# Performance work log

Hardware: AMD Instinct MI355X
Metric: run time of the kernel (lower is better)

## Reference

```python
import jax, jax.numpy as jnp
import numpy as np

HEADS = 8
DIM_HEAD = 64
EPS = 1e-4


def softmax_kernel(data, proj, is_query):
    # data: [b,h,n,d], proj: [m,d]
    data_normalizer = data.shape[-1] ** -0.25
    ratio = proj.shape[0] ** -0.5
    data_dash = jnp.einsum('bhnd,md->bhnm', data_normalizer * data, proj)
    diag = (data * data).sum(-1) * 0.5 * (data_normalizer ** 2)  # [b,h,n]
    diag = diag[..., None]
    if is_query:
        stab = jnp.max(data_dash, axis=-1, keepdims=True)
    else:
        stab = jnp.max(data_dash)
    return ratio * (jnp.exp(data_dash - diag - stab) + EPS)


def linear_attention(q, k, v):
    # q,k: [b,h,n,m], v: [b,h,n,e]
    k_cumsum = k.sum(axis=-2)  # [b,h,m]
    d_inv = 1.0 / jnp.einsum('bhnm,bhm->bhn', q, k_cumsum)
    context = jnp.einsum('bhnm,bhne->bhme', k, v)  # [b,h,m,e]
    return jnp.einsum('bhme,bhnm,bhn->bhne', context, q, d_inv)


def setup_inputs() -> dict:
    key = jax.random.key(0)
    ks = jax.random.split(key, 6)
    b, n, dim = 8, 4096, 512
    m, dh = 266, DIM_HEAD
    x = jax.random.normal(ks[0], (b, n, dim), dtype=jnp.float32)
    s = dim ** -0.5
    Wq = jax.random.normal(ks[1], (dim, dim), dtype=jnp.float32) * s
    Wk = jax.random.normal(ks[2], (dim, dim), dtype=jnp.float32) * s
    Wv = jax.random.normal(ks[3], (dim, dim), dtype=jnp.float32) * s
    Wo = jax.random.normal(ks[4], (dim, dim), dtype=jnp.float32) * s
    bo = jnp.zeros((dim,), dtype=jnp.float32)
    proj = jax.random.normal(ks[5], (m, dh), dtype=jnp.float32)
    return {"x": x, "Wq": Wq, "Wk": Wk, "Wv": Wv, "Wo": Wo, "bo": bo, "proj": proj}


def reference(x, Wq, Wk, Wv, Wv_unused=None, *, _=None, **__):
    raise NotImplementedError


def reference(x, Wq, Wk, Wv, Wo, bo, proj):
    b, n, dim = x.shape
    h, dh = HEADS, DIM_HEAD
    # Linear projections (weights stored as [in, out])
    q = (x @ Wq).reshape(b, n, h, dh).transpose(0, 2, 1, 3)  # [b,h,n,dh]
    k = (x @ Wk).reshape(b, n, h, dh).transpose(0, 2, 1, 3)
    v = (x @ Wv).reshape(b, n, h, dh).transpose(0, 2, 1, 3)
    qp = softmax_kernel(q, proj, is_query=True)   # [b,h,n,m]
    kp = softmax_kernel(k, proj, is_query=False)  # [b,h,n,m]
    out = linear_attention(qp, kp, v)             # [b,h,n,dh]
    out = out.transpose(0, 2, 1, 3).reshape(b, n, h * dh)
    return out @ Wo + bo
```

## Files before the change

kernel.cpp:

```cpp
#include <hip/hip_runtime.h>
#include <stdint.h>

#define B_ 8
#define N_ 4096
#define H_ 8
#define DH_ 64
#define DIM_ 512
#define M_ 266
#define MP_ 320
#define BH_ 64
#define BNROWS_ 32768
#define CN_ 0.35355339059327373f
#define RATIO_ 0.06131393394849658f
#define EPS_ 1e-4f
#define REPS_ (RATIO_ * EPS_)

typedef __bf16 bf16x8 __attribute__((ext_vector_type(8)));
typedef float f32x4 __attribute__((ext_vector_type(4)));

union U8 { bf16x8 v; uint4 u; uint2 u2[2]; uint16_t s[8]; };

__device__ __forceinline__ uint32_t f2bf(float f) {
  uint32_t u = __float_as_uint(f);
  u += 0x7FFFu + ((u >> 16) & 1u);
  return u >> 16;
}
__device__ __forceinline__ uint32_t pkbf(float a, float b) {
  uint32_t r;
  asm("v_cvt_pk_bf16_f32 %0, %1, %2" : "=v"(r) : "v"(a), "v"(b));
  return r;
}
__device__ __forceinline__ float bflo(uint32_t u) { return __uint_as_float(u << 16); }
__device__ __forceinline__ float bfhi(uint32_t u) { return __uint_as_float(u & 0xFFFF0000u); }
__device__ __forceinline__ void unp8(uint4 u, float* f) {
  f[0] = bflo(u.x); f[1] = bfhi(u.x); f[2] = bflo(u.y); f[3] = bfhi(u.y);
  f[4] = bflo(u.z); f[5] = bfhi(u.z); f[6] = bflo(u.w); f[7] = bfhi(u.w);
}
__device__ __forceinline__ float f4get(const float4& v, int i) {
  return ((const float*)&v)[i];
}
__device__ __forceinline__ uint32_t fenc(float f) {
  uint32_t u = __float_as_uint(f);
  return u ^ ((uint32_t)((int32_t)u >> 31) | 0x80000000u);
}
__device__ __forceinline__ float fdec(uint32_t e) {
  uint32_t u = (e & 0x80000000u) ? (e ^ 0x80000000u) : ~e;
  return __uint_as_float(u);
}
__device__ __forceinline__ int piperm(int p) {
  int tmt = p >> 4, r = p & 15;
  return 32 * (tmt >> 1) + 8 * (r >> 2) + 4 * (tmt & 1) + (r & 3);
}
__device__ __forceinline__ int phinv(int r) {
  int lo = r & 15;
  return 8 * (lo >> 2) + (lo & 3) + ((r >> 4) << 2);
}
__device__ __forceinline__ void glds16(const uint16_t* g, uint16_t* l) {
  __builtin_amdgcn_global_load_lds(
      (const __attribute__((address_space(1))) void*)g,
      (__attribute__((address_space(3))) void*)l, 16, 0, 0);
}

__global__ void init_stab(uint32_t* s) { *s = fenc(-3.4e38f); }

__global__ __launch_bounds__(256) void cast_x(const float* __restrict__ x,
                                              uint16_t* __restrict__ xb, int n4) {
  int i = blockIdx.x * 256 + threadIdx.x;
  if (i >= n4) return;
  float4 v = ((const float4*)x)[i];
  uint2 o;
  o.x = f2bf(v.x) | (f2bf(v.y) << 16);
  o.y = f2bf(v.z) | (f2bf(v.w) << 16);
  ((uint2*)xb)[i] = o;
}

__global__ __launch_bounds__(256) void cast_wt(const float* __restrict__ w,
                                               uint16_t* __restrict__ wt) {
  int i = blockIdx.x * 256 + threadIdx.x;
  int k = i >> 9, n = i & 511;
  wt[(size_t)n * 512 + k] = (uint16_t)f2bf(w[i]);
}

__global__ __launch_bounds__(256) void cast_projb(const float* __restrict__ proj,
                                                  uint16_t* __restrict__ projb) {
  int i = blockIdx.x * 256 + threadIdx.x;
  if (i >= MP_ * DH_) return;
  int p = i >> 6, d = i & 63;
  int pi = piperm(p);
  float v = (pi < M_) ? proj[pi * DH_ + d] : 0.f;
  projb[i] = (uint16_t)f2bf(v);
}

template <int EPI>
__global__ __launch_bounds__(256) void gemm_glds(const uint16_t* __restrict__ A,
                                                 const uint16_t* __restrict__ Bt,
                                                 float* __restrict__ outF,
                                                 const float* __restrict__ bias,
                                                 uint16_t* __restrict__ qb,
                                                 uint16_t* __restrict__ kbuf,
                                                 uint16_t* __restrict__ vTb) {
  __shared__ __align__(16) uint16_t As[2][128 * 32];
  __shared__ __align__(16) uint16_t Bs[2][128 * 32];
  const int t = threadIdx.x, lane = t & 63, w = t >> 6;
  const int g = lane >> 4, r16 = lane & 15;
  const int wr = (w >> 1) * 64, wc = (w & 1) * 64;
  const size_t rowA0 = (size_t)blockIdx.x * 128;
  const size_t rowB0 = (size_t)blockIdx.y * 128;
  const int K = 512;

  f32x4 acc[4][4];
#pragma unroll
  for (int i = 0; i < 4; ++i)
#pragma unroll
    for (int j = 0; j < 4; ++j) acc[i][j] = (f32x4){0.f, 0.f, 0.f, 0.f};

  auto stageG = [&](int kt, int buf) {
#pragma unroll
    for (int s = 0; s < 2; ++s) {
      const int row = w * 32 + s * 16;
      const uint16_t* ga = A + (rowA0 + row + (lane >> 2)) * (size_t)K + kt * 32 + (lane & 3) * 8;
      glds16(ga, &As[buf][row * 32]);
      const uint16_t* gb = Bt + (rowB0 + row + (lane >> 2)) * (size_t)K + kt * 32 + (lane & 3) * 8;
      glds16(gb, &Bs[buf][row * 32]);
    }
  };
  stageG(0, 0);
  for (int kt = 0; kt < 16; ++kt) {
    __syncthreads();
    if (kt + 1 < 16) stageG(kt + 1, (kt + 1) & 1);
    const uint16_t* as = As[kt & 1];
    const uint16_t* bs = Bs[kt & 1];
    bf16x8 af[4], bfr[4];
#pragma unroll
    for (int i = 0; i < 4; ++i)
      af[i] = *(const bf16x8*)&as[(wr + i * 16 + r16) * 32 + g * 8];
#pragma unroll
    for (int j = 0; j < 4; ++j)
      bfr[j] = *(const bf16x8*)&bs[(wc + j * 16 + r16) * 32 + g * 8];
#pragma unroll
    for (int i = 0; i < 4; ++i)
#pragma unroll
      for (int j = 0; j < 4; ++j)
        acc[i][j] = __builtin_amdgcn_mfma_f32_16x16x32_bf16(af[i], bfr[j], acc[i][j], 0, 0, 0);
  }
  const int region = blockIdx.y >> 2;
  const int lcolBase = (blockIdx.y & 3) * 128;
#pragma unroll
  for (int i = 0; i < 4; ++i) {
    const size_t row0 = rowA0 + wr + i * 16 + g * 4;
#pragma unroll
    for (int j = 0; j < 4; ++j) {
      if constexpr (EPI == 0) {
        const size_t col = rowB0 + wc + j * 16 + r16;
        float badd = bias ? bias[col] : 0.f;
#pragma unroll
        for (int q = 0; q < 4; ++q)
          outF[(row0 + q) * (size_t)512 + col] = acc[i][j][q] + badd;
      } else {
        const int lcol = lcolBase + wc + j * 16 + r16;
        if (region == 2) {
          int bb = (int)(row0 >> 12), n = (int)(row0 & 4095);
          int hh = lcol >> 6, e = lcol & 63;
          uint2 o;
          o.x = pkbf(acc[i][j][0], acc[i][j][1]);
          o.y = pkbf(acc[i][j][2], acc[i][j][3]);
          *(uint2*)&vTb[((size_t)((bb * 8 + hh) * 64 + e)) * 4096 + n] = o;
        } else {
          uint16_t* dst = region ? kbuf : qb;
#pragma unroll
          for (int q = 0; q < 4; ++q)
            dst[(row0 + q) * (size_t)512 + lcol] = (uint16_t)f2bf(acc[i][j][q]);
        }
      }
    }
  }
}

#define GKP_ 40
template <bool AF32, bool CBF16, bool VT>
__global__ __launch_bounds__(256) void gemm_k(const void* __restrict__ Av,
                                              const uint16_t* __restrict__ Bt,
                                              void* __restrict__ Cv,
                                              const float* __restrict__ bias,
                                              int Ndim, int Kdim, int lda) {
  __shared__ uint16_t As[2][128 * GKP_];
  __shared__ uint16_t Bs[2][128 * GKP_];
  const int t = threadIdx.x;
  const int lane = t & 63;
  const int wave = t >> 6;
  const int wr = (wave >> 1) * 64, wc = (wave & 1) * 64;
  const int g = lane >> 4, r16 = lane & 15;
  const int srow = t >> 2;
  const int skk = (t & 3) * 8;
  const size_t rowA0 = (size_t)blockIdx.x * 128;
  const size_t rowB0 = (size_t)blockIdx.y * 128;

  f32x4 acc[4][4];
#pragma unroll
  for (int i = 0; i < 4; ++i)
#pragma unroll
    for (int j = 0; j < 4; ++j) acc[i][j] = (f32x4){0.f, 0.f, 0.f, 0.f};

  const int NK = Kdim >> 5;
  auto stage = [&](int kt, int buf) {
    uint4 a0, a1;
    if constexpr (AF32) {
      const float* ga = (const float*)Av + (rowA0 + srow) * (size_t)lda + kt * 32 + skk;
      float4 x0 = *(const float4*)ga;
      float4 x1 = *(const float4*)(ga + 4);
      float4 y0 = *(const float4*)(ga + 64 * (size_t)lda);
      float4 y1 = *(const float4*)(ga + 64 * (size_t)lda + 4);
      a0.x = f2bf(x0.x) | (f2bf(x0.y) << 16);
      a0.y = f2bf(x0.z) | (f2bf(x0.w) << 16);
      a0.z = f2bf(x1.x) | (f2bf(x1.y) << 16);
      a0.w = f2bf(x1.z) | (f2bf(x1.w) << 16);
      a1.x = f2bf(y0.x) | (f2bf(y0.y) << 16);
      a1.y = f2bf(y0.z) | (f2bf(y0.w) << 16);
      a1.z = f2bf(y1.x) | (f2bf(y1.y) << 16);
      a1.w = f2bf(y1.z) | (f2bf(y1.w) << 16);
    } else {
      const uint16_t* ga = (const uint16_t*)Av + (rowA0 + srow) * (size_t)lda + kt * 32 + skk;
      a0 = *(const uint4*)ga;
      a1 = *(const uint4*)(ga + 64 * (size_t)lda);
    }
    const uint16_t* gb = Bt + (rowB0 + srow) * (size_t)Kdim + kt * 32 + skk;
    uint4 b0 = *(const uint4*)gb;
    uint4 b1 = *(const uint4*)(gb + 64 * (size_t)Kdim);
    *(uint4*)&As[buf][srow * GKP_ + skk] = a0;
    *(uint4*)&As[buf][(srow + 64) * GKP_ + skk] = a1;
    *(uint4*)&Bs[buf][srow * GKP_ + skk] = b0;
    *(uint4*)&Bs[buf][(srow + 64) * GKP_ + skk] = b1;
  };
  stage(0, 0);
  for (int kt = 0; kt < NK; ++kt) {
    __syncthreads();
    if (kt + 1 < NK) stage(kt + 1, (kt + 1) & 1);
    const uint16_t* as = As[kt & 1];
    const uint16_t* bs = Bs[kt & 1];
    bf16x8 af[4], bfr[4];
#pragma unroll
    for (int i = 0; i < 4; ++i)
      af[i] = *(const bf16x8*)&as[(wr + i * 16 + r16) * GKP_ + g * 8];
#pragma unroll
    for (int j = 0; j < 4; ++j)
      bfr[j] = *(const bf16x8*)&bs[(wc + j * 16 + r16) * GKP_ + g * 8];
#pragma unroll
    for (int i = 0; i < 4; ++i)
#pragma unroll
      for (int j = 0; j < 4; ++j)
        acc[i][j] = __builtin_amdgcn_mfma_f32_16x16x32_bf16(af[i], bfr[j], acc[i][j], 0, 0, 0);
  }
#pragma unroll
  for (int i = 0; i < 4; ++i) {
    const size_t row0 = rowA0 + wr + i * 16 + g * 4;
#pragma unroll
    for (int j = 0; j < 4; ++j) {
      const size_t col = rowB0 + wc + j * 16 + r16;
      if constexpr (VT) {
        int bb = (int)(row0 >> 12), n = (int)(row0 & 4095);
        int hh = (int)(col >> 6), e = (int)(col & 63);
        uint2 o;
        o.x = pkbf(acc[i][j][0], acc[i][j][1]);
        o.y = pkbf(acc[i][j][2], acc[i][j][3]);
        *(uint2*)&((uint16_t*)Cv)[((size_t)((bb * 8 + hh) * 64 + e)) * 4096 + n] = o;
      } else {
        float badd = bias ? bias[col] : 0.f;
#pragma unroll
        for (int q = 0; q < 4; ++q) {
          float val = acc[i][j][q] + badd;
          if constexpr (CBF16)
            ((uint16_t*)Cv)[(row0 + q) * (size_t)Ndim + col] = (uint16_t)f2bf(val);
          else
            ((float*)Cv)[(row0 + q) * (size_t)Ndim + col] = val;
        }
      }
    }
  }
}

__global__ __launch_bounds__(256) void stab2_mfma(const uint16_t* __restrict__ kb,
                                                  const uint16_t* __restrict__ projb,
                                                  uint32_t* __restrict__ stab) {
  __shared__ uint16_t kt[2][32][72];
  __shared__ float wred[4];
  const int t = threadIdx.x, lane = t & 63, w = t >> 6;
  const int g = lane >> 4, r16 = lane & 15;
  const int bh = blockIdx.x, ns = blockIdx.y;
  const int b = bh >> 3, h = bh & 7;
  bf16x8 pj[5][2];
  bool mval[5];
#pragma unroll
  for (int mt = 0; mt < 5; ++mt) {
    int m16 = mt * 64 + w * 16;
    pj[mt][0] = *(const bf16x8*)&projb[(m16 + r16) * 64 + g * 8];
    pj[mt][1] = *(const bf16x8*)&projb[(m16 + r16) * 64 + 32 + g * 8];
    mval[mt] = piperm(m16 + r16) < M_;
  }
  auto stage = [&](int it, int buf) {
    int n0 = ns * 256 + it * 32;
    int row = t >> 3, c8 = t & 7;
    *(uint4*)&kt[buf][row][c8 * 8] =
        *(const uint4*)&kb[((size_t)(b * N_ + n0 + row)) * DIM_ + h * DH_ + c8 * 8];
  };
  stage(0, 0);
  __syncthreads();
  float vmax = -3.4e38f;
  for (int it = 0; it < 8; ++it) {
    int cur = it & 1;
    if (it + 1 < 8) stage(it + 1, cur ^ 1);
    bf16x8 ka[2][2];
#pragma unroll
    for (int nsub = 0; nsub < 2; ++nsub) {
      ka[nsub][0] = *(const bf16x8*)&kt[cur][nsub * 16 + r16][g * 8];
      ka[nsub][1] = *(const bf16x8*)&kt[cur][nsub * 16 + r16][32 + g * 8];
    }
#pragma unroll
    for (int mt = 0; mt < 5; ++mt) {
#pragma unroll
      for (int nsub = 0; nsub < 2; ++nsub) {
        f32x4 c4 = (f32x4){0.f, 0.f, 0.f, 0.f};
        c4 = __builtin_amdgcn_mfma_f32_16x16x32_bf16(ka[nsub][0], pj[mt][0], c4, 0, 0, 0);
        c4 = __builtin_amdgcn_mfma_f32_16x16x32_bf16(ka[nsub][1], pj[mt][1], c4, 0, 0, 0);
        if (mval[mt])
          vmax = fmaxf(vmax, fmaxf(fmaxf(c4[0], c4[1]), fmaxf(c4[2], c4[3])));
      }
    }
    __syncthreads();
  }
#pragma unroll
  for (int off = 32; off; off >>= 1) vmax = fmaxf(vmax, __shfl_xor(vmax, off));
  if (lane == 0) wred[w] = vmax;
  __syncthreads();
  if (t == 0) {
    float m = fmaxf(fmaxf(wred[0], wred[1]), fmaxf(wred[2], wred[3]));
    atomicMax(stab, fenc(CN_ * m));
  }
}

__global__ __launch_bounds__(256) void ctx_mfma(const uint16_t* __restrict__ kb,
                                                const uint16_t* __restrict__ vTb,
                                                const uint16_t* __restrict__ projb,
                                                const uint32_t* __restrict__ stab_e,
                                                float* __restrict__ ctxp,
                                                float* __restrict__ kcump,
                                                int iters) {
  __shared__ uint16_t kt[2][32][72];
  __shared__ uint16_t vt[2][64][40];
  __shared__ float dk2[2][32];
  __shared__ uint16_t kpb[4][16][40];
  const int t = threadIdx.x, lane = t & 63, w = t >> 6;
  const int g = lane >> 4, r16 = lane & 15;
  const int mt = blockIdx.x, bh = blockIdx.y, ns = blockIdx.z;
  const int b = bh >> 3, h = bh & 7;
  const int m16 = mt * 64 + w * 16;
  const float stab = fdec(*stab_e);
  const bool mvalid = piperm(m16 + r16) < M_;
  bf16x8 pj0 = *(const bf16x8*)&projb[(m16 + r16) * 64 + g * 8];
  bf16x8 pj1 = *(const bf16x8*)&projb[(m16 + r16) * 64 + 32 + g * 8];

  auto stage = [&](int it, int buf) {
    int n0 = (ns * iters + it) * 32;
    {
      int row = t >> 3, c8 = t & 7;
      uint4 kv = *(const uint4*)&kb[((size_t)(b * N_ + n0 + row)) * DIM_ + h * DH_ + c8 * 8];
      *(uint4*)&kt[buf][row][c8 * 8] = kv;
      float f[8]; unp8(kv, f);
      float sq = f[0]*f[0]+f[1]*f[1]+f[2]*f[2]+f[3]*f[3]+f[4]*f[4]+f[5]*f[5]+f[6]*f[6]+f[7]*f[7];
      sq += __shfl_xor(sq, 1); sq += __shfl_xor(sq, 2); sq += __shfl_xor(sq, 4);
      if (c8 == 0) dk2[buf][row] = 0.5f * CN_ * CN_ * sq;
    }
    {
      int e = t >> 2, c = t & 3;
      uint4 vv = *(const uint4*)&vTb[((size_t)(bh * 64 + e)) * 4096 + n0 + c * 8];
      *(uint4*)&vt[buf][e][c * 8] = vv;
    }
  };
  f32x4 acc[4];
#pragma unroll
  for (int j = 0; j < 4; ++j) acc[j] = (f32x4){0.f, 0.f, 0.f, 0.f};
  float kcacc = 0.f;

  stage(0, 0);
  __syncthreads();
  for (int it = 0; it < iters; ++it) {
    int cur = it & 1;
    if (it + 1 < iters) stage(it + 1, cur ^ 1);
#pragma unroll
    for (int nsub = 0; nsub < 2; ++nsub) {
      bf16x8 ka0 = *(const bf16x8*)&kt[cur][nsub * 16 + r16][g * 8];
      bf16x8 ka1 = *(const bf16x8*)&kt[cur][nsub * 16 + r16][32 + g * 8];
      f32x4 c4 = (f32x4){0.f, 0.f, 0.f, 0.f};
      c4 = __builtin_amdgcn_mfma_f32_16x16x32_bf16(ka0, pj0, c4, 0, 0, 0);
      c4 = __builtin_amdgcn_mfma_f32_16x16x32_bf16(ka1, pj1, c4, 0, 0, 0);
      float4 dkv = *(const float4*)&dk2[cur][nsub * 16 + 4 * g];
      float kp[4];
#pragma unroll
      for (int q = 0; q < 4; ++q) {
        float arg = CN_ * c4[q] - f4get(dkv, q) - stab;
        float e = RATIO_ * __expf(arg) + REPS_;
        kp[q] = mvalid ? e : 0.f;
        kcacc += kp[q];
      }
      *(uint2*)&kpb[w][r16][nsub * 16 + 4 * g] = make_uint2(pkbf(kp[0], kp[1]), pkbf(kp[2], kp[3]));
    }
    U8 kq; kq.u = *(const uint4*)&kpb[w][r16][g * 8];
#pragma unroll
    for (int j = 0; j < 4; ++j) {
      U8 vf; vf.u = *(const uint4*)&vt[cur][j * 16 + r16][g * 8];
      acc[j] = __builtin_amdgcn_mfma_f32_16x16x32_bf16(kq.v, vf.v, acc[j], 0, 0, 0);
    }
    __syncthreads();
  }
#pragma unroll
  for (int j = 0; j < 4; ++j) {
    float4 o = make_float4(acc[j][0], acc[j][1], acc[j][2], acc[j][3]);
    *(float4*)&ctxp[(((size_t)ns * BH_ + bh) * 64 + j * 16 + r16) * MP_ + m16 + 4 * g] = o;
  }
  kcacc += __shfl_xor(kcacc, 16);
  kcacc += __shfl_xor(kcacc, 32);
  if (lane < 16) kcump[((size_t)ns * BH_ + bh) * MP_ + m16 + lane] = kcacc;
}

__global__ __launch_bounds__(256) void merge_kernel(const float* __restrict__ ctxp,
                                                    const float* __restrict__ kcump,
                                                    uint16_t* __restrict__ ctxgb,
                                                    float* __restrict__ kcumg,
                                                    int nsp) {
  int idx = blockIdx.x * 256 + threadIdx.x;
  const int total = BH_ * 64 * MP_;
  if (idx < total) {
    float s = 0.f;
    for (int p = 0; p < nsp; ++p) s += ctxp[(size_t)p * total + idx];
    int row = idx / MP_;
    int pos = idx - row * MP_;
    int col = (pos & ~31) + phinv(pos & 31);
    ctxgb[(size_t)row * MP_ + col] = (uint16_t)f2bf(s);
  }
  const int ktotal = BH_ * MP_;
  if (idx < ktotal) {
    float s = 0.f;
    for (int p = 0; p < nsp; ++p) s += kcump[(size_t)p * ktotal + idx];
    kcumg[idx] = s;
  }
}

__global__ __launch_bounds__(512) void attn_mfma(const uint16_t* __restrict__ qb,
                                                 const uint16_t* __restrict__ projb,
                                                 const uint16_t* __restrict__ ctxgb,
                                                 const float* __restrict__ kcumg,
                                                 uint16_t* __restrict__ attnb) {
  __shared__ uint16_t ctile[64][328];
  __shared__ uint16_t qs[128][72];
  __shared__ float kcums[MP_];
  __shared__ float dqs[128];
  __shared__ float denb[8][16];
  const int t = threadIdx.x, lane = t & 63, w = t >> 6;
  const int g = lane >> 4, r16 = lane & 15;
  const int nch = blockIdx.x, bh = blockIdx.y;
  const int b = bh >> 3, h = bh & 7;
  {
    int row = t >> 3, cb = t & 7;
#pragma unroll
    for (int cc = 0; cc < 5; ++cc) {
      int cN = cb * 40 + cc * 8;
      *(uint4*)&ctile[row][cN] = *(const uint4*)&ctxgb[((size_t)bh * 64 + row) * MP_ + cN];
    }
  }
  if (t < MP_) kcums[t] = kcumg[(size_t)bh * MP_ + t];

  for (int it = 0; it < 4; ++it) {
    const int nbase = nch * 512 + it * 128;
    __syncthreads();
    {
      int row = t >> 2, c2 = t & 3;
      float sq = 0.f;
#pragma unroll
      for (int cc = 0; cc < 2; ++cc) {
        int c8 = c2 * 2 + cc;
        uint4 qv = *(const uint4*)&qb[((size_t)(b * N_ + nbase + row)) * DIM_ + h * DH_ + c8 * 8];
        *(uint4*)&qs[row][c8 * 8] = qv;
        float f[8]; unp8(qv, f);
        sq += f[0]*f[0]+f[1]*f[1]+f[2]*f[2]+f[3]*f[3]+f[4]*f[4]+f[5]*f[5]+f[6]*f[6]+f[7]*f[7];
      }
      sq += __shfl_xor(sq, 1); sq += __shfl_xor(sq, 2);
      if (c2 == 0) dqs[row] = 0.5f * CN_ * CN_ * sq;
    }
    __syncthreads();
    bf16x8 qf0 = *(const bf16x8*)&qs[w * 16 + r16][g * 8];
    bf16x8 qf1 = *(const bf16x8*)&qs[w * 16 + r16][32 + g * 8];
    f32x4 S[18];
#pragma unroll
    for (int mt = 0; mt < 18; ++mt) {
      bf16x8 pa0 = *(const bf16x8*)&projb[(mt * 16 + r16) * 64 + g * 8];
      bf16x8 pa1 = *(const bf16x8*)&projb[(mt * 16 + r16) * 64 + 32 + g * 8];
      f32x4 c4 = (f32x4){0.f, 0.f, 0.f, 0.f};
      c4 = __builtin_amdgcn_mfma_f32_16x16x32_bf16(pa0, qf0, c4, 0, 0, 0);
      S[mt] = __builtin_amdgcn_mfma_f32_16x16x32_bf16(pa1, qf1, c4, 0, 0, 0);
    }
    float rmax = -3.4e38f;
#pragma unroll
    for (int mt = 0; mt < 18; ++mt) {
#pragma unroll
      for (int q = 0; q < 4; ++q) {
        bool val = (mt < 16) || (256 + 4 * (mt & 1) + 8 * g + q < M_);
        if (val) rmax = fmaxf(rmax, CN_ * S[mt][q]);
      }
    }
    rmax = fmaxf(rmax, __shfl_xor(rmax, 16));
    rmax = fmaxf(rmax, __shfl_xor(rmax, 32));
    const float offv = rmax + dqs[w * 16 + r16];
    float denp = 0.f;
    uint32_t pk[18][2];
#pragma unroll
    for (int mt = 0; mt < 18; ++mt) {
      float4 kc4 = *(const float4*)&kcums[mt * 16 + 4 * g];
      float qp[4];
#pragma unroll
      for (int q = 0; q < 4; ++q) {
        bool val = (mt < 16) || (256 + 4 * (mt & 1) + 8 * g + q < M_);
        float e = RATIO_ * __expf(CN_ * S[mt][q] - offv) + REPS_;
        qp[q] = val ? e : 0.f;
        denp += qp[q] * f4get(kc4, q);
      }
      pk[mt][0] = pkbf(qp[0], qp[1]);
      pk[mt][1] = pkbf(qp[2], qp[3]);
    }
    denp += __shfl_xor(denp, 16);
    denp += __shfl_xor(denp, 32);
    if (lane < 16) denb[w][lane] = denp;
    f32x4 o[4];
#pragma unroll
    for (int j = 0; j < 4; ++j) o[j] = (f32x4){0.f, 0.f, 0.f, 0.f};
#pragma unroll
    for (int s = 0; s < 9; ++s) {
      U8 af; af.u = make_uint4(pk[2 * s][0], pk[2 * s][1], pk[2 * s + 1][0], pk[2 * s + 1][1]);
#pragma unroll
      for (int j = 0; j < 4; ++j) {
        U8 cf; cf.u = *(const uint4*)&ctile[j * 16 + r16][s * 32 + g * 8];
        o[j] = __builtin_amdgcn_mfma_f32_16x16x32_bf16(af.v, cf.v, o[j], 0, 0, 0);
      }
    }
    float4 dv = *(const float4*)&denb[w][4 * g];
    float rd[4];
#pragma unroll
    for (int q = 0; q < 4; ++q) rd[q] = 1.0f / f4get(dv, q);
#pragma unroll
    for (int j = 0; j < 4; ++j) {
#pragma unroll
      for (int q = 0; q < 4; ++q) {
        float val = o[j][q] * rd[q];
        int n = nbase + w * 16 + 4 * g + q;
        attnb[((size_t)(b * N_ + n)) * DIM_ + h * DH_ + j * 16 + r16] = (uint16_t)f2bf(val);
      }
    }
  }
}

extern "C" void kernel_launch(void* const* d_in, const int* in_sizes, int n_in,
                              void* d_out, int out_size, void* d_ws, size_t ws_size,
                              hipStream_t stream) {
  const float* x = (const float*)d_in[0];
  const float* Wq = (const float*)d_in[1];
  const float* Wk = (const float*)d_in[2];
  const float* Wv = (const float*)d_in[3];
  const float* Wo = (const float*)d_in[4];
  const float* bo = (const float*)d_in[5];
  const float* proj = (const float*)d_in[6];
  float* out = (float*)d_out;

  const bool tierA = ws_size >= (size_t)95000000;
  const int NS = (tierA || ws_size >= (size_t)61000000) ? 4 : 2;

  char* ws = (char*)d_ws;
  size_t off = 0;
  auto alloc = [&](size_t bytes) {
    char* p = ws + off;
    off += (bytes + 255) & ~(size_t)255;
    return p;
  };
  uint16_t* wqkvT = (uint16_t*)alloc((size_t)1536 * 512 * 2);
  uint16_t* woT = (uint16_t*)alloc((size_t)512 * 512 * 2);
  uint16_t* projb = (uint16_t*)alloc((size_t)MP_ * DH_ * 2);
  uint16_t* vTb = (uint16_t*)alloc((size_t)BNROWS_ * DIM_ * 2);
  float* ctxp = (float*)alloc((size_t)NS * BH_ * 64 * MP_ * 4);
  float* kcump = (float*)alloc((size_t)NS * BH_ * MP_ * 4);
  uint16_t* ctxgb = (uint16_t*)alloc((size_t)BH_ * 64 * MP_ * 2);
  float* kcumg = (float*)alloc((size_t)BH_ * MP_ * 4);
  uint32_t* stab = (uint32_t*)alloc(256);
  uint16_t* xb = tierA ? (uint16_t*)alloc((size_t)BNROWS_ * DIM_ * 2) : nullptr;
  uint16_t* qb = (uint16_t*)d_out;
  uint16_t* kb = qb + (size_t)BNROWS_ * DIM_;
  uint16_t* attnb = vTb;

  init_stab<<<1, 1, 0, stream>>>(stab);
  cast_wt<<<1024, 256, 0, stream>>>(Wq, wqkvT);
  cast_wt<<<1024, 256, 0, stream>>>(Wk, wqkvT + (size_t)512 * 512);
  cast_wt<<<1024, 256, 0, stream>>>(Wv, wqkvT + (size_t)1024 * 512);
  cast_wt<<<1024, 256, 0, stream>>>(Wo, woT);
  cast_projb<<<80, 256, 0, stream>>>(proj, projb);

  if (tierA) {
    cast_x<<<16384, 256, 0, stream>>>(x, xb, BNROWS_ * DIM_ / 4);
    gemm_glds<1><<<dim3(256, 12), 256, 0, stream>>>(xb, wqkvT, nullptr, nullptr, qb, kb, vTb);
  } else {
    dim3 gg(256, 4);
    gemm_k<true, true, false><<<gg, 256, 0, stream>>>(x, wqkvT, qb, nullptr, 512, 512, 512);
    gemm_k<true, true, false><<<gg, 256, 0, stream>>>(x, wqkvT + (size_t)512 * 512, kb, nullptr, 512, 512, 512);
    gemm_k<true, false, true><<<gg, 256, 0, stream>>>(x, wqkvT + (size_t)1024 * 512, vTb, nullptr, 512, 512, 512);
  }

  stab2_mfma<<<dim3(64, 16), 256, 0, stream>>>(kb, projb, stab);
  ctx_mfma<<<dim3(5, 64, NS), 256, 0, stream>>>(kb, vTb, projb, stab, ctxp, kcump, 128 / NS);
  merge_kernel<<<5120, 256, 0, stream>>>(ctxp, kcump, ctxgb, kcumg, NS);
  attn_mfma<<<dim3(8, 64), 512, 0, stream>>>(qb, projb, ctxgb, kcumg, attnb);
  gemm_k<false, false, false><<<dim3(256, 4), 256, 0, stream>>>(attnb, woT, out, bo, 512, 512, 512);
}
```

Before: 303.1 us.

## Remap GEMM blocks per XCD, raise split count, store partial contexts in bf16

The QKV GEMM now launches as a flat grid that is remapped so each XCD gets a contiguous band of row tiles, for better L2 locality. The output projection switches from the register-staged gemm_k to the direct global-to-LDS gemm_glds kernel. The workspace-tier fallback is removed so the x-cast plus fused GEMM path always runs. The ctx split count goes up to 8, and stab2 is split finer, for more parallelism. Partial contexts are stored in bf16 to halve merge traffic, at the cost of extra rounding in the partial sums.

Result: slower. 313.1 us (+3.3%).

```diff
diff --git a/kernel.cpp b/kernel.cpp
--- a/kernel.cpp
+++ b/kernel.cpp
@@ -10,6 +10,7 @@
 #define MP_ 320
 #define BH_ 64
 #define BNROWS_ 32768
+#define NS_ 8
 #define CN_ 0.35355339059327373f
 #define RATIO_ 0.06131393394849658f
 #define EPS_ 1e-4f
@@ -104,8 +105,12 @@
   const int t = threadIdx.x, lane = t & 63, w = t >> 6;
   const int g = lane >> 4, r16 = lane & 15;
   const int wr = (w >> 1) * 64, wc = (w & 1) * 64;
-  const size_t rowA0 = (size_t)blockIdx.x * 128;
-  const size_t rowB0 = (size_t)blockIdx.y * 128;
+  const int flat = blockIdx.x;
+  const int xcd = flat & 7, jj = flat >> 3;
+  const int bx = xcd * 32 + (jj & 31);
+  const int by = jj >> 5;
+  const size_t rowA0 = (size_t)bx * 128;
+  const size_t rowB0 = (size_t)by * 128;
   const int K = 512;
 
   f32x4 acc[4][4];
@@ -143,8 +148,8 @@
       for (int j = 0; j < 4; ++j)
         acc[i][j] = __builtin_amdgcn_mfma_f32_16x16x32_bf16(af[i], bfr[j], acc[i][j], 0, 0, 0);
   }
-  const int region = blockIdx.y >> 2;
-  const int lcolBase = (blockIdx.y & 3) * 128;
+  const int region = by >> 2;
+  const int lcolBase = (by & 3) * 128;
 #pragma unroll
   for (int i = 0; i < 4; ++i) {
     const size_t row0 = rowA0 + wr + i * 16 + g * 4;
@@ -176,108 +181,6 @@
   }
 }
 
-#define GKP_ 40
-template <bool AF32, bool CBF16, bool VT>
-__global__ __launch_bounds__(256) void gemm_k(const void* __restrict__ Av,
-                                              const uint16_t* __restrict__ Bt,
-                                              void* __restrict__ Cv,
-                                              const float* __restrict__ bias,
-                                              int Ndim, int Kdim, int lda) {
-  __shared__ uint16_t As[2][128 * GKP_];
-  __shared__ uint16_t Bs[2][128 * GKP_];
-  const int t = threadIdx.x;
-  const int lane = t & 63;
-  const int wave = t >> 6;
-  const int wr = (wave >> 1) * 64, wc = (wave & 1) * 64;
-  const int g = lane >> 4, r16 = lane & 15;
-  const int srow = t >> 2;
-  const int skk = (t & 3) * 8;
-  const size_t rowA0 = (size_t)blockIdx.x * 128;
-  const size_t rowB0 = (size_t)blockIdx.y * 128;
-
-  f32x4 acc[4][4];
-#pragma unroll
-  for (int i = 0; i < 4; ++i)
-#pragma unroll
-    for (int j = 0; j < 4; ++j) acc[i][j] = (f32x4){0.f, 0.f, 0.f, 0.f};
-
-  const int NK = Kdim >> 5;
-  auto stage = [&](int kt, int buf) {
-    uint4 a0, a1;
-    if constexpr (AF32) {
-      const float* ga = (const float*)Av + (rowA0 + srow) * (size_t)lda + kt * 32 + skk;
-      float4 x0 = *(const float4*)ga;
-      float4 x1 = *(const float4*)(ga + 4);
-      float4 y0 = *(const float4*)(ga + 64 * (size_t)lda);
-      float4 y1 = *(const float4*)(ga + 64 * (size_t)lda + 4);
-      a0.x = f2bf(x0.x) | (f2bf(x0.y) << 16);
-      a0.y = f2bf(x0.z) | (f2bf(x0.w) << 16);
-      a0.z = f2bf(x1.x) | (f2bf(x1.y) << 16);
-      a0.w = f2bf(x1.z) | (f2bf(x1.w) << 16);
-      a1.x = f2bf(y0.x) | (f2bf(y0.y) << 16);
-      a1.y = f2bf(y0.z) | (f2bf(y0.w) << 16);
-      a1.z = f2bf(y1.x) | (f2bf(y1.y) << 16);
-      a1.w = f2bf(y1.z) | (f2bf(y1.w) << 16);
-    } else {
-      const uint16_t* ga = (const uint16_t*)Av + (rowA0 + srow) * (size_t)lda + kt * 32 + skk;
-      a0 = *(const uint4*)ga;
-      a1 = *(const uint4*)(ga + 64 * (size_t)lda);
-    }
-    const uint16_t* gb = Bt + (rowB0 + srow) * (size_t)Kdim + kt * 32 + skk;
-    uint4 b0 = *(const uint4*)gb;
-    uint4 b1 = *(const uint4*)(gb + 64 * (size_t)Kdim);
-    *(uint4*)&As[buf][srow * GKP_ + skk] = a0;
-    *(uint4*)&As[buf][(srow + 64) * GKP_ + skk] = a1;
-    *(uint4*)&Bs[buf][srow * GKP_ + skk] = b0;
-    *(uint4*)&Bs[buf][(srow + 64) * GKP_ + skk] = b1;
-  };
-  stage(0, 0);
-  for (int kt = 0; kt < NK; ++kt) {
-    __syncthreads();
-    if (kt + 1 < NK) stage(kt + 1, (kt + 1) & 1);
-    const uint16_t* as = As[kt & 1];
-    const uint16_t* bs = Bs[kt & 1];
-    bf16x8 af[4], bfr[4];
-#pragma unroll
-    for (int i = 0; i < 4; ++i)
-      af[i] = *(const bf16x8*)&as[(wr + i * 16 + r16) * GKP_ + g * 8];
-#pragma unroll
-    for (int j = 0; j < 4; ++j)
-      bfr[j] = *(const bf16x8*)&bs[(wc + j * 16 + r16) * GKP_ + g * 8];
-#pragma unroll
-    for (int i = 0; i < 4; ++i)
-#pragma unroll
-      for (int j = 0; j < 4; ++j)
-        acc[i][j] = __builtin_amdgcn_mfma_f32_16x16x32_bf16(af[i], bfr[j], acc[i][j], 0, 0, 0);
-  }
-#pragma unroll
-  for (int i = 0; i < 4; ++i) {
-    const size_t row0 = rowA0 + wr + i * 16 + g * 4;
-#pragma unroll
-    for (int j = 0; j < 4; ++j) {
-      const size_t col = rowB0 + wc + j * 16 + r16;
-      if constexpr (VT) {
-        int bb = (int)(row0 >> 12), n = (int)(row0 & 4095);
-        int hh = (int)(col >> 6), e = (int)(col & 63);
-        uint2 o;
-        o.x = pkbf(acc[i][j][0], acc[i][j][1]);
-        o.y = pkbf(acc[i][j][2], acc[i][j][3]);
-        *(uint2*)&((uint16_t*)Cv)[((size_t)((bb * 8 + hh) * 64 + e)) * 4096 + n] = o;
-      } else {
-        float badd = bias ? bias[col] : 0.f;
-#pragma unroll
-        for (int q = 0; q < 4; ++q) {
-          float val = acc[i][j][q] + badd;
-          if constexpr (CBF16)
-            ((uint16_t*)Cv)[(row0 + q) * (size_t)Ndim + col] = (uint16_t)f2bf(val);
-          else
-            ((float*)Cv)[(row0 + q) * (size_t)Ndim + col] = val;
-        }
-      }
-    }
-  }
-}
-
 __global__ __launch_bounds__(256) void stab2_mfma(const uint16_t* __restrict__ kb,
                                                   const uint16_t* __restrict__ projb,
                                                   uint32_t* __restrict__ stab) {
@@ -297,7 +200,7 @@
     mval[mt] = piperm(m16 + r16) < M_;
   }
   auto stage = [&](int it, int buf) {
-    int n0 = ns * 256 + it * 32;
+    int n0 = ns * 128 + it * 32;
     int row = t >> 3, c8 = t & 7;
     *(uint4*)&kt[buf][row][c8 * 8] =
         *(const uint4*)&kb[((size_t)(b * N_ + n0 + row)) * DIM_ + h * DH_ + c8 * 8];
@@ -305,9 +208,9 @@
   stage(0, 0);
   __syncthreads();
   float vmax = -3.4e38f;
-  for (int it = 0; it < 8; ++it) {
+  for (int it = 0; it < 4; ++it) {
     int cur = it & 1;
-    if (it + 1 < 8) stage(it + 1, cur ^ 1);
+    if (it + 1 < 4) stage(it + 1, cur ^ 1);
     bf16x8 ka[2][2];
 #pragma unroll
     for (int nsub = 0; nsub < 2; ++nsub) {
@@ -341,9 +244,8 @@
                                                 const uint16_t* __restrict__ vTb,
                                                 const uint16_t* __restrict__ projb,
                                                 const uint32_t* __restrict__ stab_e,
-                                                float* __restrict__ ctxp,
-                                                float* __restrict__ kcump,
-                                                int iters) {
+                                                uint16_t* __restrict__ ctxpb,
+                                                float* __restrict__ kcump) {
   __shared__ uint16_t kt[2][32][72];
   __shared__ uint16_t vt[2][64][40];
   __shared__ float dk2[2][32];
@@ -357,6 +259,7 @@
   const bool mvalid = piperm(m16 + r16) < M_;
   bf16x8 pj0 = *(const bf16x8*)&projb[(m16 + r16) * 64 + g * 8];
   bf16x8 pj1 = *(const bf16x8*)&projb[(m16 + r16) * 64 + 32 + g * 8];
+  const int iters = 4096 / (32 * NS_);
 
   auto stage = [&](int it, int buf) {
     int n0 = (ns * iters + it) * 32;
@@ -413,24 +316,27 @@
   }
 #pragma unroll
   for (int j = 0; j < 4; ++j) {
-    float4 o = make_float4(acc[j][0], acc[j][1], acc[j][2], acc[j][3]);
-    *(float4*)&ctxp[(((size_t)ns * BH_ + bh) * 64 + j * 16 + r16) * MP_ + m16 + 4 * g] = o;
+    uint2 o;
+    o.x = pkbf(acc[j][0], acc[j][1]);
+    o.y = pkbf(acc[j][2], acc[j][3]);
+    *(uint2*)&ctxpb[(((size_t)ns * BH_ + bh) * 64 + j * 16 + r16) * MP_ + m16 + 4 * g] = o;
   }
   kcacc += __shfl_xor(kcacc, 16);
   kcacc += __shfl_xor(kcacc, 32);
   if (lane < 16) kcump[((size_t)ns * BH_ + bh) * MP_ + m16 + lane] = kcacc;
 }
 
-__global__ __launch_bounds__(256) void merge_kernel(const float* __restrict__ ctxp,
+__global__ __launch_bounds__(256) void merge_kernel(const uint16_t* __restrict__ ctxpb,
                                                     const float* __restrict__ kcump,
                                                     uint16_t* __restrict__ ctxgb,
-                                                    float* __restrict__ kcumg,
-                                                    int nsp) {
+                                                    float* __restrict__ kcumg) {
   int idx = blockIdx.x * 256 + threadIdx.x;
   const int total = BH_ * 64 * MP_;
   if (idx < total) {
     float s = 0.f;
-    for (int p = 0; p < nsp; ++p) s += ctxp[(size_t)p * total + idx];
+#pragma unroll
+    for (int p = 0; p < NS_; ++p)
+      s += __uint_as_float((uint32_t)ctxpb[(size_t)p * total + idx] << 16);
     int row = idx / MP_;
     int pos = idx - row * MP_;
     int col = (pos & ~31) + phinv(pos & 31);
@@ -439,7 +345,8 @@
   const int ktotal = BH_ * MP_;
   if (idx < ktotal) {
     float s = 0.f;
-    for (int p = 0; p < nsp; ++p) s += kcump[(size_t)p * ktotal + idx];
+#pragma unroll
+    for (int p = 0; p < NS_; ++p) s += kcump[(size_t)p * ktotal + idx];
     kcumg[idx] = s;
   }
 }
@@ -568,9 +475,6 @@
   const float* proj = (const float*)d_in[6];
   float* out = (float*)d_out;
 
-  const bool tierA = ws_size >= (size_t)95000000;
-  const int NS = (tierA || ws_size >= (size_t)61000000) ? 4 : 2;
-
   char* ws = (char*)d_ws;
   size_t off = 0;
   auto alloc = [&](size_t bytes) {
@@ -582,12 +486,12 @@
   uint16_t* woT = (uint16_t*)alloc((size_t)512 * 512 * 2);
   uint16_t* projb = (uint16_t*)alloc((size_t)MP_ * DH_ * 2);
   uint16_t* vTb = (uint16_t*)alloc((size_t)BNROWS_ * DIM_ * 2);
-  float* ctxp = (float*)alloc((size_t)NS * BH_ * 64 * MP_ * 4);
-  float* kcump = (float*)alloc((size_t)NS * BH_ * MP_ * 4);
+  uint16_t* ctxpb = (uint16_t*)alloc((size_t)NS_ * BH_ * 64 * MP_ * 2);
+  float* kcump = (float*)alloc((size_t)NS_ * BH_ * MP_ * 4);
   uint16_t* ctxgb = (uint16_t*)alloc((size_t)BH_ * 64 * MP_ * 2);
   float* kcumg = (float*)alloc((size_t)BH_ * MP_ * 4);
   uint32_t* stab = (uint32_t*)alloc(256);
-  uint16_t* xb = tierA ? (uint16_t*)alloc((size_t)BNROWS_ * DIM_ * 2) : nullptr;
+  uint16_t* xb = (uint16_t*)alloc((size_t)BNROWS_ * DIM_ * 2);
   uint16_t* qb = (uint16_t*)d_out;
   uint16_t* kb = qb + (size_t)BNROWS_ * DIM_;
   uint16_t* attnb = vTb;
@@ -598,20 +502,13 @@
   cast_wt<<<1024, 256, 0, stream>>>(Wv, wqkvT + (size_t)1024 * 512);
   cast_wt<<<1024, 256, 0, stream>>>(Wo, woT);
   cast_projb<<<80, 256, 0, stream>>>(proj, projb);
-
-  if (tierA) {
-    cast_x<<<16384, 256, 0, stream>>>(x, xb, BNROWS_ * DIM_ / 4);
-    gemm_glds<1><<<dim3(256, 12), 256, 0, stream>>>(xb, wqkvT, nullptr, nullptr, qb, kb, vTb);
-  } else {
-    dim3 gg(256, 4);
-    gemm_k<true, true, false><<<gg, 256, 0, stream>>>(x, wqkvT, qb, nullptr, 512, 512, 512);
-    gemm_k<true, true, false><<<gg, 256, 0, stream>>>(x, wqkvT + (size_t)512 * 512, kb, nullptr, 512, 512, 512);
-    gemm_k<true, false, true><<<gg, 256, 0, stream>>>(x, wqkvT + (size_t)1024 * 512, vTb, nullptr, 512, 512, 512);
-  }
-
-  stab2_mfma<<<dim3(64, 16), 256, 0, stream>>>(kb, projb, stab);
-  ctx_mfma<<<dim3(5, 64, NS), 256, 0, stream>>>(kb, vTb, projb, stab, ctxp, kcump, 128 / NS);
-  merge_kernel<<<5120, 256, 0, stream>>>(ctxp, kcump, ctxgb, kcumg, NS);
+  cast_x<<<16384, 256, 0, stream>>>(x, xb, BNROWS_ * DIM_ / 4);
+
+  gemm_glds<1><<<3072, 256, 0, stream>>>(xb, wqkvT, nullptr, nullptr, qb, kb, vTb);
+
+  stab2_mfma<<<dim3(64, 32), 256, 0, stream>>>(kb, projb, stab);
+  ctx_mfma<<<dim3(5, 64, NS_), 256, 0, stream>>>(kb, vTb, projb, stab, ctxpb, kcump);
+  merge_kernel<<<5120, 256, 0, stream>>>(ctxpb, kcump, ctxgb, kcumg);
   attn_mfma<<<dim3(8, 64), 512, 0, stream>>>(qb, projb, ctxgb, kcumg, attnb);
-  gemm_k<false, false, false><<<dim3(256, 4), 256, 0, stream>>>(attnb, woT, out, bo, 512, 512, 512);
-}
+  gemm_glds<0><<<1024, 256, 0, stream>>>(attnb, woT, out, bo, nullptr, nullptr, nullptr);
+}
```
